# Optimization experiments

Hardware: AMD Instinct MI355X
Metric: run time of the kernel (lower is better)

## Reference

```python
import jax, jax.numpy as jnp
import numpy as np

# static config (matches init_kwargs)
B, CIN, L = 32, 128, 4096
COUT, K = 256, 5
PAD_SIZE = 2
INPUT_SCALE = 0.05
OUTPUT_SCALE = 0.1
INPUT_ZP = -3
OUTPUT_ZP = -128
QMIN, QMAX = -128, 127  # 8-bit signed range


def setup_inputs() -> dict:
    key = jax.random.key(0)
    k1, k2, k3, k4 = jax.random.split(key, 4)
    x = jax.random.normal(k1, (B, CIN, L), dtype=jnp.float32)
    weight = jax.random.randint(k2, (COUT, CIN, K), -127, 128, dtype=jnp.int32).astype(jnp.int8)
    # shifted quantized bias (int32), plausible magnitude
    bias = jax.random.randint(k3, (COUT,), -20000, 20000, dtype=jnp.int32)
    # per-output-channel weight scale
    weight_scale = jax.random.uniform(k4, (COUT,), dtype=jnp.float32, minval=1e-3, maxval=1e-2)
    return {"x": x, "weight": weight, "bias": bias, "weight_scale": weight_scale}


def reference(x, weight, bias, weight_scale):
    # --- linear_quantize (first_layer) ---
    xq = jnp.round(x / INPUT_SCALE) + INPUT_ZP
    xq = jnp.clip(xq, QMIN, QMAX).astype(jnp.int8)
    # --- ReplicationPad1d(pad_size) ---
    xq = jnp.pad(xq, ((0, 0), (0, 0), (PAD_SIZE, PAD_SIZE)), mode="edge")
    # --- int8 conv1d with int32 accumulation ---
    acc = jax.lax.conv_general_dilated(
        xq.astype(jnp.int32), weight.astype(jnp.int32),
        window_strides=(1,), padding=[(0, 0)],
        dimension_numbers=("NCH", "OIH", "NCH"))  # [B, COUT, Lout]
    acc = acc + bias[None, :, None]
    # --- per-channel requantization ---
    scale = (INPUT_SCALE * weight_scale / OUTPUT_SCALE)[None, :, None]
    out = acc.astype(jnp.float32) * scale + OUTPUT_ZP
    out = jnp.clip(jnp.round(out), QMIN, QMAX).astype(jnp.int8)
    return out
```

## Files before the change

### kernel.cpp

```cpp
#include <hip/hip_runtime.h>


#define B_    32
#define CIN   128
#define LEN   4096
#define COUT  256
#define KW    5
#define TROWS 136

#define WTF_BYTES (KW * 2 * 16 * 64 * 16)

typedef int          i32x4 __attribute__((ext_vector_type(4)));
typedef signed char  s8;

__device__ __forceinline__ s8 quant_i8(float xv) {
    float q = rintf(xv * 20.0f) - 3.0f;
    q = fminf(fmaxf(q, -128.0f), 127.0f);
    return (s8)(int)q;
}

__global__ __launch_bounds__(256) void wprep_kernel(
        const int* __restrict__ w, const int* __restrict__ bias,
        const float* __restrict__ wscale,
        s8* __restrict__ wtf, float* __restrict__ tbl)
{
    int o    = blockIdx.x * 256 + threadIdx.x;
    int lane = o & 63, frag = o >> 6;
    int k    = frag >> 5;
    int s    = (frag >> 4) & 1;
    int co   = ((frag & 15) << 4) + (lane & 15);
    int ci   = (s << 6) + ((lane >> 4) << 4);
    union { s8 c[16]; i32x4 v; } q;
    #pragma unroll
    for (int j = 0; j < 16; ++j)
        q.c[j] = (s8)w[co * (CIN * KW) + (ci + j) * KW + k];
    *(i32x4*)(wtf + (size_t)frag * 1024 + lane * 16) = q.v;

    if (blockIdx.x == 0) {
        int c = threadIdx.x;
        float sc = __fdiv_rn(__fmul_rn(0.05f, wscale[c]), 0.1f);
        tbl[c]       = sc;
        tbl[256 + c] = fmaf((float)bias[c], sc, -128.0f);
    }
}

__global__ __launch_bounds__(512, 4) void conv_fused(
        const float* __restrict__ x, const s8* __restrict__ wtf,
        const float* __restrict__ tbl, int* __restrict__ out)
{
    __shared__ __align__(16) s8 smem[TROWS * CIN];

    int orig  = (blockIdx.x & 7) * 128 + (blockIdx.x >> 3);
    int ltile = orig & 31;
    int b     = orig >> 5;
    int l0    = ltile << 7;
    int tid   = threadIdx.x;
    int wid   = tid >> 6, lane = tid & 63;
    int lr    = lane & 15, lh = lane >> 4;
    int cog   = (wid & 3) << 6;
    int wl    = (wid >> 2) << 6;

    const float* xb = x + (size_t)b * CIN * LEN;

    for (int p = wid; p < 24; p += 8) {
        int row = ((p >> 3) << 6) + lane;
        int c   = p & 7;
        if (row < TROWS) {
            int gl = l0 - 4 + row;
            gl = min(max(gl, 0), LEN - 1);
            const float* src = xb + (size_t)(c << 4) * LEN + gl;
            union { s8 cc[16]; i32x4 v; } q;
            #pragma unroll
            for (int j = 0; j < 16; ++j)
                q.cc[j] = quant_i8(src[(size_t)j * LEN]);
            *(i32x4*)(smem + (row << 7) + ((c ^ (row & 7)) << 4)) = q.v;
        }
    }
    __syncthreads();

    i32x4 acc[4][4] = {};
    #pragma unroll
    for (int k = 0; k < KW; ++k) {
        #pragma unroll
        for (int s = 0; s < 2; ++s) {
            i32x4 af[4];
            #pragma unroll
            for (int ct = 0; ct < 4; ++ct)
                af[ct] = *(const i32x4*)(
                    wtf + (size_t)((k << 5) + (s << 4) + (cog >> 4) + ct) * 1024 + lane * 16);
            i32x4 bf[4];
            int chunk = (s << 2) + lh;
            #pragma unroll
            for (int lt = 0; lt < 4; ++lt) {
                int row = wl + (lt << 4) + lr + k + 2;
                bf[lt] = *(const i32x4*)(smem + (row << 7) + ((chunk ^ (row & 7)) << 4));
            }
            #pragma unroll
            for (int ct = 0; ct < 4; ++ct)
                #pragma unroll
                for (int lt = 0; lt < 4; ++lt)
                    acc[ct][lt] = __builtin_amdgcn_mfma_i32_16x16x64_i8(
                        bf[lt], af[ct], acc[ct][lt], 0, 0, 0);
        }
    }

    size_t outb = (size_t)b * COUT * LEN;
    #pragma unroll
    for (int ct = 0; ct < 4; ++ct) {
        int co = cog + (ct << 4) + lr;
        float scv = tbl[co];
        float off = tbl[256 + co];
        int* orow = out + outb + (size_t)co * LEN + l0 + wl + (lh << 2);
        #pragma unroll
        for (int lt = 0; lt < 4; ++lt) {
            i32x4 pk;
            #pragma unroll
            for (int r = 0; r < 4; ++r) {
                float o = rintf(fmaf((float)acc[ct][lt][r], scv, off));
                o = fminf(fmaxf(o, -128.0f), 127.0f);
                pk[r] = (int)o;
            }
            *(i32x4*)(orow + (lt << 4)) = pk;
        }
    }
}

extern "C" void kernel_launch(void* const* d_in, const int* in_sizes, int n_in,
                              void* d_out, int out_size, void* d_ws, size_t ws_size,
                              hipStream_t stream)
{
    const float* x    = (const float*)d_in[0];
    const int*   w    = (const int*)d_in[1];
    const int*   bias = (const int*)d_in[2];
    const float* wsc  = (const float*)d_in[3];
    int* out = (int*)d_out;

    s8*    wtf = (s8*)d_ws;
    float* tbl = (float*)((char*)d_ws + WTF_BYTES);

    wprep_kernel<<<dim3(40), dim3(256), 0, stream>>>(w, bias, wsc, wtf, tbl);
    conv_fused<<<dim3(1024), dim3(512), 0, stream>>>(x, wtf, tbl, out);
}
```

Before: 56.04 us.

## Loop over L sub-tiles per block with double-buffered LDS and register prefetch

Each block now covers a 256-wide L segment and walks it in eight 32-wide tiles instead of handling one 128-wide tile. LDS is double-buffered: the next tile's x values are loaded into registers during the current tile's MFMAs, then quantized into the other buffer. Weight fragments for three of the five taps, plus the scale/offset values, stay in registers across tiles, and the grid is halved. This aims to overlap global loads with compute and to cut repeated weight fetches, at the cost of a larger halo fraction per tile, fewer resident blocks, and more register pressure.

```diff
diff --git a/kernel.cpp b/kernel.cpp
--- a/kernel.cpp
+++ b/kernel.cpp
@@ -6,7 +6,9 @@
 #define LEN   4096
 #define COUT  256
 #define KW    5
-#define TROWS 136
+#define TROWS 40
+#define NT    8
+#define LDS_TILE 5120
 
 #define WTF_BYTES (KW * 2 * 16 * 64 * 16)
 
@@ -14,7 +16,7 @@
 typedef signed char  s8;
 
 __device__ __forceinline__ s8 quant_i8(float xv) {
-    float q = rintf(xv * 20.0f) - 3.0f;
+    float q = rintf(fmaf(xv, 20.0f, -3.0f));
     q = fminf(fmaxf(q, -128.0f), 127.0f);
     return (s8)(int)q;
 }
@@ -48,79 +50,121 @@
         const float* __restrict__ x, const s8* __restrict__ wtf,
         const float* __restrict__ tbl, int* __restrict__ out)
 {
-    __shared__ __align__(16) s8 smem[TROWS * CIN];
+    __shared__ __align__(16) s8 smem[2 * LDS_TILE];
 
-    int orig  = (blockIdx.x & 7) * 128 + (blockIdx.x >> 3);
-    int ltile = orig & 31;
-    int b     = orig >> 5;
-    int l0    = ltile << 7;
-    int tid   = threadIdx.x;
-    int wid   = tid >> 6, lane = tid & 63;
-    int lr    = lane & 15, lh = lane >> 4;
-    int cog   = (wid & 3) << 6;
-    int wl    = (wid >> 2) << 6;
+    int orig = (blockIdx.x & 7) * 64 + (blockIdx.x >> 3);
+    int lseg = orig & 15;
+    int b    = orig >> 4;
+    int L0   = lseg << 8;
+    int tid  = threadIdx.x;
+    int wid  = tid >> 6, lane = tid & 63;
+    int lr   = lane & 15, lh = lane >> 4;
+    int cog  = wid << 5;
 
-    const float* xb = x + (size_t)b * CIN * LEN;
+    const float* xb  = x + (size_t)b * CIN * LEN;
+    const float* src = xb + (size_t)(wid << 4) * LEN;
 
-    for (int p = wid; p < 24; p += 8) {
-        int row = ((p >> 3) << 6) + lane;
-        int c   = p & 7;
-        if (row < TROWS) {
-            int gl = l0 - 4 + row;
-            gl = min(max(gl, 0), LEN - 1);
-            const float* src = xb + (size_t)(c << 4) * LEN + gl;
-            union { s8 cc[16]; i32x4 v; } q;
+    i32x4 afr[12];
+    #pragma unroll
+    for (int k = 0; k < 3; ++k)
+        #pragma unroll
+        for (int s = 0; s < 2; ++s)
             #pragma unroll
-            for (int j = 0; j < 16; ++j)
-                q.cc[j] = quant_i8(src[(size_t)j * LEN]);
-            *(i32x4*)(smem + (row << 7) + ((c ^ (row & 7)) << 4)) = q.v;
-        }
+            for (int ct = 0; ct < 2; ++ct)
+                afr[(k * 2 + s) * 2 + ct] = *(const i32x4*)(
+                    wtf + (size_t)((k << 5) + (s << 4) + wid * 2 + ct) * 1024 + lane * 16);
+
+    float sc0 = tbl[cog + lr],      off0 = tbl[256 + cog + lr];
+    float sc1 = tbl[cog + 16 + lr], off1 = tbl[256 + cog + 16 + lr];
+
+    if (lane < TROWS) {
+        int gl = min(max(L0 - 4 + lane, 0), LEN - 1);
+        union { s8 cc[16]; i32x4 v; } q;
+        #pragma unroll
+        for (int j = 0; j < 16; ++j)
+            q.cc[j] = quant_i8(src[(size_t)j * LEN + gl]);
+        *(i32x4*)(smem + (lane << 7) + ((wid ^ (lane & 7)) << 4)) = q.v;
     }
     __syncthreads();
 
-    i32x4 acc[4][4] = {};
-    #pragma unroll
-    for (int k = 0; k < KW; ++k) {
+    size_t outb = (size_t)b * COUT * LEN;
+
+    for (int t = 0; t < NT; ++t) {
+        int Lt = L0 + (t << 5);
+        s8* buf  = smem + (t & 1) * LDS_TILE;
+        s8* nbuf = smem + ((t & 1) ^ 1) * LDS_TILE;
+
+        i32x4 af3[4];
         #pragma unroll
-        for (int s = 0; s < 2; ++s) {
-            i32x4 af[4];
+        for (int s = 0; s < 2; ++s)
             #pragma unroll
-            for (int ct = 0; ct < 4; ++ct)
-                af[ct] = *(const i32x4*)(
-                    wtf + (size_t)((k << 5) + (s << 4) + (cog >> 4) + ct) * 1024 + lane * 16);
-            i32x4 bf[4];
-            int chunk = (s << 2) + lh;
+            for (int ct = 0; ct < 2; ++ct)
+                af3[s * 2 + ct] = *(const i32x4*)(
+                    wtf + (size_t)((3 << 5) + (s << 4) + wid * 2 + ct) * 1024 + lane * 16);
+
+        float vf[16];
+        bool morel = (t + 1 < NT) && (lane < TROWS);
+        int gln = min(max(Lt + 28 + lane, 0), LEN - 1);
+        if (morel) {
             #pragma unroll
-            for (int lt = 0; lt < 4; ++lt) {
-                int row = wl + (lt << 4) + lr + k + 2;
-                bf[lt] = *(const i32x4*)(smem + (row << 7) + ((chunk ^ (row & 7)) << 4));
+            for (int j = 0; j < 16; ++j)
+                vf[j] = src[(size_t)j * LEN + gln];
+        }
+
+        i32x4 acc[2][2] = {};
+        i32x4 af4[4];
+        #pragma unroll
+        for (int k = 0; k < KW; ++k) {
+            if (k == 4) {
+                #pragma unroll
+                for (int s = 0; s < 2; ++s)
+                    #pragma unroll
+                    for (int ct = 0; ct < 2; ++ct)
+                        af4[s * 2 + ct] = *(const i32x4*)(
+                            wtf + (size_t)((4 << 5) + (s << 4) + wid * 2 + ct) * 1024 + lane * 16);
             }
             #pragma unroll
-            for (int ct = 0; ct < 4; ++ct)
+            for (int s = 0; s < 2; ++s) {
+                i32x4 a0, a1;
+                if (k < 3)      { a0 = afr[(k * 2 + s) * 2]; a1 = afr[(k * 2 + s) * 2 + 1]; }
+                else if (k == 3){ a0 = af3[s * 2];           a1 = af3[s * 2 + 1]; }
+                else            { a0 = af4[s * 2];           a1 = af4[s * 2 + 1]; }
+                int chunk = (s << 2) + lh;
                 #pragma unroll
-                for (int lt = 0; lt < 4; ++lt)
-                    acc[ct][lt] = __builtin_amdgcn_mfma_i32_16x16x64_i8(
-                        bf[lt], af[ct], acc[ct][lt], 0, 0, 0);
+                for (int lt = 0; lt < 2; ++lt) {
+                    int row = (lt << 4) + lr + k + 2;
+                    i32x4 bf = *(const i32x4*)(buf + (row << 7) + ((chunk ^ (row & 7)) << 4));
+                    acc[0][lt] = __builtin_amdgcn_mfma_i32_16x16x64_i8(bf, a0, acc[0][lt], 0, 0, 0);
+                    acc[1][lt] = __builtin_amdgcn_mfma_i32_16x16x64_i8(bf, a1, acc[1][lt], 0, 0, 0);
+                }
+            }
         }
-    }
 
-    size_t outb = (size_t)b * COUT * LEN;
-    #pragma unroll
-    for (int ct = 0; ct < 4; ++ct) {
-        int co = cog + (ct << 4) + lr;
-        float scv = tbl[co];
-        float off = tbl[256 + co];
-        int* orow = out + outb + (size_t)co * LEN + l0 + wl + (lh << 2);
+        if (morel) {
+            union { s8 cc[16]; i32x4 v; } q;
+            #pragma unroll
+            for (int j = 0; j < 16; ++j) q.cc[j] = quant_i8(vf[j]);
+            *(i32x4*)(nbuf + (lane << 7) + ((wid ^ (lane & 7)) << 4)) = q.v;
+        }
+        __syncthreads();
+
         #pragma unroll
-        for (int lt = 0; lt < 4; ++lt) {
-            i32x4 pk;
+        for (int ct = 0; ct < 2; ++ct) {
+            float scv = ct ? sc1 : sc0;
+            float off = ct ? off1 : off0;
+            int co = cog + (ct << 4) + lr;
+            int* orow = out + outb + (size_t)co * LEN + Lt + (lh << 2);
             #pragma unroll
-            for (int r = 0; r < 4; ++r) {
-                float o = rintf(fmaf((float)acc[ct][lt][r], scv, off));
-                o = fminf(fmaxf(o, -128.0f), 127.0f);
-                pk[r] = (int)o;
+            for (int lt = 0; lt < 2; ++lt) {
+                i32x4 pk;
+                #pragma unroll
+                for (int r = 0; r < 4; ++r) {
+                    float o = rintf(fmaf((float)acc[ct][lt][r], scv, off));
+                    o = fminf(fmaxf(o, -128.0f), 127.0f);
+                    pk[r] = (int)o;
+                }
+                *(i32x4*)(orow + (lt << 4)) = pk;
             }
-            *(i32x4*)(orow + (lt << 4)) = pk;
         }
     }
 }
@@ -139,5 +183,5 @@
     float* tbl = (float*)((char*)d_ws + WTF_BYTES);
 
     wprep_kernel<<<dim3(40), dim3(256), 0, stream>>>(w, bias, wsc, wtf, tbl);
-    conv_fused<<<dim3(1024), dim3(512), 0, stream>>>(x, wtf, tbl, out);
+    conv_fused<<<dim3(512), dim3(512), 0, stream>>>(x, wtf, tbl, out);
 }
```

Measured after the change: 124.4 us. 122% more time.
